# Performance work log

Measured on AMD Instinct MI355X. Metric: run time of the kernel, lower is better.

The kernel has to match this reference:

```python
import jax, jax.numpy as jnp
from jax import lax
import numpy as np

B, N, H, T, NPB = 1024, 50, 128, 50, 3
C_TANH, NEG = 10.0, 1e9


def _lstm(x, h, c, Wi, Wh, b):
    gates = x @ Wi + h @ Wh + b
    i, f, g, o = jnp.split(gates, 4, axis=-1)
    c2 = jax.nn.sigmoid(f) * c + jax.nn.sigmoid(i) * jnp.tanh(g)
    return jax.nn.sigmoid(o) * jnp.tanh(c2), c2


def setup_inputs() -> dict:
    key = jax.random.key(0)
    ks = jax.random.split(key, 20)
    rn = lambda k, shape, fan: (jax.random.normal(k, shape, jnp.float32) / np.float32(np.sqrt(fan)))
    return {
        'input_pnt': jax.random.uniform(ks[0], (B, N, 2), jnp.float32),
        'W_emb': rn(ks[1], (2, H), 2), 'b_emb': jnp.zeros((H,), jnp.float32),
        'dec_init': rn(ks[2], (1, 1, H), H),
        'Wi': rn(ks[3], (H, 4 * H), H), 'Wh': rn(ks[4], (H, 4 * H), H), 'b_lstm': jnp.zeros((4 * H,), jnp.float32),
        'Wq_g': rn(ks[5], (H, H), H), 'Wref_g': rn(ks[6], (H, H), H), 'v_g': rn(ks[7], (H,), H),
        'Wq_p': rn(ks[8], (H, H), H), 'Wref_p': rn(ks[9], (H, H), H), 'v_p': rn(ks[10], (H,), H),
        'Wi_c': rn(ks[11], (H, 4 * H), H), 'Wh_c': rn(ks[12], (H, 4 * H), H), 'b_c': jnp.zeros((4 * H,), jnp.float32),
        'Wq_c': rn(ks[13], (H, H), H), 'Wref_c': rn(ks[14], (H, H), H), 'v_c': rn(ks[15], (H,), H),
        'W1': rn(ks[16], (H, H), H), 'b1': jnp.zeros((H,), jnp.float32),
        'W2': rn(ks[17], (H, 1), H), 'b2': jnp.zeros((1,), jnp.float32),
    }


def _forward(input_pnt, W_emb, b_emb, dec_init, Wi, Wh, b_lstm, Wq_g, Wref_g, v_g,
             Wq_p, Wref_p, v_p, Wi_c, Wh_c, b_c, Wq_c, Wref_c, v_c, W1, b1, W2, b2):
    context = input_pnt @ W_emb + b_emb                    # [B,N,H] embedded nodes
    e_g = context @ Wref_g                                  # glimpse keys (step-invariant, hoisted)
    e_p = context @ Wref_p                                  # pointer keys (hoisted)
    z = jnp.zeros((B, H), context.dtype)
    carry0 = (z, z, jnp.zeros((B, N), context.dtype), jnp.broadcast_to(dec_init[0, 0], (B, H)))

    def step(carry, _):
        h, c, mask, dec_in = carry
        h2, c2 = _lstm(dec_in, h, c, Wi, Wh, b_lstm)
        # glimpse attention (masked)
        q = h2 @ Wq_g
        u = jnp.einsum('bnh,h->bn', jnp.tanh(e_g + q[:, None, :]), v_g) - NEG * mask
        g = jnp.einsum('bn,bnh->bh', jax.nn.softmax(u, -1), e_g)
        # pointer attention with tanh exploration clipping (masked)
        u2 = jnp.einsum('bnh,h->bn', jnp.tanh(e_p + (g @ Wq_p)[:, None, :]), v_p)
        logit = C_TANH * jnp.tanh(u2) - NEG * mask
        logprob = jax.nn.log_softmax(logit, -1)
        prob = jax.nn.softmax(logit, -1)
        action = jnp.argmax(prob, -1)                       # greedy decode
        mask2 = jnp.maximum(mask, jax.nn.one_hot(action, N, dtype=mask.dtype))
        dec_next = jnp.take_along_axis(context, action[:, None, None], axis=1)[:, 0]
        coords = jnp.take_along_axis(input_pnt, action[:, None, None], axis=1)[:, 0]
        return (h2, c2, mask2, dec_next), (logprob, prob, action, coords)

    (_, _, _, dec_last), (logprobs, probs, actions, coords) = lax.scan(step, carry0, None, length=T)
    logprobs = jnp.transpose(logprobs, (1, 0, 2))           # [B,T,N]
    probs = jnp.transpose(probs, (1, 0, 2))
    actions = jnp.transpose(actions, (1, 0))                # [B,T]
    coords = jnp.transpose(coords, (1, 0, 2))               # [B,T,2] visited coordinates
    # reward: TSP tour length
    seg = coords[:, 1:] - coords[:, :-1]
    close = coords[:, 0] - coords[:, -1]
    R = jnp.sum(jnp.sqrt(jnp.sum(seg * seg, -1) + 1e-10), -1) + jnp.sqrt(jnp.sum(close * close, -1) + 1e-10)
    # critic: one LSTM step on last action broadcast to hidden, cn[0], then process blocks
    a4c = jnp.broadcast_to(actions[:, -1].astype(context.dtype)[:, None], (B, H))
    _, hy = _lstm(a4c, z, z, Wi_c, Wh_c, b_c)
    enc = dec_last[:, None, :]                              # context gathered at last action, [B,1,H]
    e_c = enc @ Wref_c
    for _ in range(NPB):
        u = jnp.einsum('bnh,h->bn', jnp.tanh(e_c + (hy @ Wq_c)[:, None, :]), v_c)
        hy = jnp.einsum('bn,bnh->bh', jax.nn.softmax(C_TANH * jnp.tanh(u), -1), e_c)
    v = (jax.nn.relu(hy @ W1 + b1) @ W2 + b2)[:, 0]
    return R, v, logprobs, actions, coords, probs


def reference(input_pnt, W_emb, b_emb, dec_init, Wi, Wh, b_lstm, Wq_g, Wref_g, v_g,
              Wq_p, Wref_p, v_p, Wi_c, Wh_c, b_c, Wq_c, Wref_c, v_c, W1, b1, W2, b2):
    return _forward(input_pnt, W_emb, b_emb, dec_init, Wi, Wh, b_lstm, Wq_g, Wref_g, v_g,
                    Wq_p, Wref_p, v_p, Wi_c, Wh_c, b_c, Wq_c, Wref_c, v_c, W1, b1, W2, b2)
```

## Files before the change

### kernel.cpp

```cpp
#include <hip/hip_runtime.h>
#include <math.h>

#define Bsz 1024
#define Npt 50
#define Hd 128
#define G4 512
#define Tt 50
#define NEGC 1000000000.0f
#define CTANH 10.0f
#define L2E 1.44269504088896340736f

#define OFF_R 0
#define OFF_V 1024
#define OFF_LP 2048
#define OFF_A 2562048
#define OFF_C 2613248
#define OFF_P 2715648

#define WS_TG 0
#define WS_TP 512
#define WS_TQ 1024
#define WS_A0 1536
#define WS_A1 2048
#define WS_A2 2560
#define WS_A3 3072
#define WS_CT 3584

typedef __attribute__((ext_vector_type(8))) short s16x8;
typedef __attribute__((ext_vector_type(4))) float fx4;

__device__ __forceinline__ float fexp2(float x) {
  float r;
  asm("v_exp_f32 %0, %1" : "=v"(r) : "v"(x));
  return r;
}

__device__ __forceinline__ float fsig(float x) {
  return __builtin_amdgcn_rcpf(1.0f + __expf(-x));
}

__device__ __forceinline__ float ftanh(float x) {
  float e = __expf(2.0f * x);
  return 1.0f - 2.0f * __builtin_amdgcn_rcpf(e + 1.0f);
}

__device__ __forceinline__ unsigned short f2bf(float x) {
  unsigned int u = __float_as_uint(x);
  unsigned int r = (u + 0x7fffu + ((u >> 16) & 1u)) >> 16;
  return (unsigned short)r;
}
__device__ __forceinline__ float bf2f(unsigned short b) {
  return __uint_as_float(((unsigned int)b) << 16);
}

__device__ __forceinline__ float dpp_sum_bcast(float x) {
  int v;
  v = __builtin_amdgcn_update_dpp(0, __float_as_int(x), 0x111, 0xf, 0xf, true);
  x += __int_as_float(v);
  v = __builtin_amdgcn_update_dpp(0, __float_as_int(x), 0x112, 0xf, 0xf, true);
  x += __int_as_float(v);
  v = __builtin_amdgcn_update_dpp(0, __float_as_int(x), 0x114, 0xf, 0xf, true);
  x += __int_as_float(v);
  v = __builtin_amdgcn_update_dpp(0, __float_as_int(x), 0x118, 0xf, 0xf, true);
  x += __int_as_float(v);
  v = __builtin_amdgcn_update_dpp(0, __float_as_int(x), 0x142, 0xf, 0xf, true);
  x += __int_as_float(v);
  v = __builtin_amdgcn_update_dpp(0, __float_as_int(x), 0x143, 0xf, 0xf, true);
  x += __int_as_float(v);
  return __int_as_float(__builtin_amdgcn_readlane(__float_as_int(x), 63));
}

__device__ __forceinline__ float dpp_max_bcast(float x) {
  int v;
  v = __builtin_amdgcn_update_dpp(0, __float_as_int(x), 0x111, 0xf, 0xf, true);
  x = fmaxf(x, __int_as_float(v));
  v = __builtin_amdgcn_update_dpp(0, __float_as_int(x), 0x112, 0xf, 0xf, true);
  x = fmaxf(x, __int_as_float(v));
  v = __builtin_amdgcn_update_dpp(0, __float_as_int(x), 0x114, 0xf, 0xf, true);
  x = fmaxf(x, __int_as_float(v));
  v = __builtin_amdgcn_update_dpp(0, __float_as_int(x), 0x118, 0xf, 0xf, true);
  x = fmaxf(x, __int_as_float(v));
  v = __builtin_amdgcn_update_dpp(0, __float_as_int(x), 0x142, 0xf, 0xf, true);
  x = fmaxf(x, __int_as_float(v));
  v = __builtin_amdgcn_update_dpp(0, __float_as_int(x), 0x143, 0xf, 0xf, true);
  x = fmaxf(x, __int_as_float(v));
  return __int_as_float(__builtin_amdgcn_readlane(__float_as_int(x), 63));
}

__device__ __forceinline__ float xsum(float x) {
  #pragma unroll
  for (int off = 32; off >= 1; off >>= 1) x += __shfl_xor(x, off, 64);
  return x;
}

__global__ __launch_bounds__(512) void k_pre(const float* __restrict__ Wemb,
                                             const float* __restrict__ bemb,
                                             const float* __restrict__ dinit,
                                             const float* __restrict__ Wi,
                                             const float* __restrict__ bl,
                                             const float* __restrict__ Wqp,
                                             const float* __restrict__ Wrg,
                                             const float* __restrict__ Wrp,
                                             const float* __restrict__ vg,
                                             const float* __restrict__ vp,
                                             const float* __restrict__ Wrc,
                                             const float* __restrict__ W1,
                                             const float* __restrict__ b1,
                                             const float* __restrict__ W2,
                                             float* __restrict__ ws) {
  __shared__ float mg_s[2][128], mp_s[2][128], cg_s[128], cp_s[128];
  __shared__ float pg_s[2][128], pc_s[128];
  __shared__ float r0_s[128], r1_s[128], rc_s[128];
  int t = threadIdx.x;
  if (t < 256) {
    int j = t >> 7, hh = t & 127;
    float ag = 0.f, ap = 0.f;
    for (int k = 0; k < 128; ++k) {
      float we = Wemb[j * 128 + k];
      ag = fmaf(we, Wrg[k * 128 + hh], ag);
      ap = fmaf(we, Wrp[k * 128 + hh], ap);
    }
    mg_s[j][hh] = ag; mp_s[j][hh] = ap;
  } else if (t < 384) {
    int hh = t & 127;
    float cgv = 0.f, cpv = 0.f;
    for (int k = 0; k < 128; ++k) {
      float be = bemb[k];
      cgv = fmaf(be, Wrg[k * 128 + hh], cgv);
      cpv = fmaf(be, Wrp[k * 128 + hh], cpv);
    }
    cg_s[hh] = cgv; cp_s[hh] = cpv;
  } else {
    int hh = t & 127;
    float a0 = 0.f, a1 = 0.f, ac = 0.f;
    for (int k = 0; k < 128; ++k) {
      float wr = Wrc[k * 128 + hh];
      a0 = fmaf(Wemb[k], wr, a0);
      a1 = fmaf(Wemb[128 + k], wr, a1);
      ac = fmaf(bemb[k], wr, ac);
    }
    r0_s[hh] = a0; r1_s[hh] = a1; rc_s[hh] = ac;
  }
  __syncthreads();
  if (t < 256) {
    int j = t >> 7, hh = t & 127;
    float pg = 0.f;
    for (int k = 0; k < 128; ++k) pg = fmaf(mg_s[j][k], Wqp[k * 128 + hh], pg);
    pg_s[j][hh] = pg;
  } else if (t < 384) {
    int hh = t & 127;
    float pcv = 0.f;
    for (int k = 0; k < 128; ++k) pcv = fmaf(cg_s[k], Wqp[k * 128 + hh], pcv);
    pc_s[hh] = pcv + cp_s[hh];
  } else {
    int hh = t & 127;
    float t0 = 0.f, t1 = 0.f, tc = 0.f;
    for (int k = 0; k < 128; ++k) {
      float w1 = W1[k * 128 + hh];
      t0 = fmaf(r0_s[k], w1, t0);
      t1 = fmaf(r1_s[k], w1, t1);
      tc = fmaf(rc_s[k], w1, tc);
    }
    float4* w4 = (float4*)ws;
    w4[WS_CT / 4 + hh] = make_float4(t0, t1, tc + b1[hh], W2[hh]);
  }
  __syncthreads();
  if (t < 128) {
    float4* w4 = (float4*)ws;
    w4[WS_TG / 4 + t] = make_float4(mg_s[0][t], mg_s[1][t], vg[t], cg_s[t]);
    w4[WS_TP / 4 + t] = make_float4(mp_s[0][t], mp_s[1][t], vp[t], cp_s[t]);
    w4[WS_TQ / 4 + t] = make_float4(pg_s[0][t], pg_s[1][t], pc_s[t], 0.f);
  }
  {
    int j = t;
    float a0 = 0.f, a1 = 0.f, a2 = 0.f, a3 = 0.f;
    for (int k = 0; k < 128; ++k) {
      float wi = Wi[k * G4 + j];
      a0 = fmaf(Wemb[k], wi, a0);
      a1 = fmaf(Wemb[128 + k], wi, a1);
      a2 = fmaf(bemb[k], wi, a2);
      a3 = fmaf(dinit[k], wi, a3);
    }
    ws[WS_A0 + j] = a0;
    ws[WS_A1 + j] = a1;
    ws[WS_A2 + j] = a2 + bl[j];
    ws[WS_A3 + j] = a3 + bl[j];
  }
}

__global__ __launch_bounds__(1024, 4) void k_mega(const float* __restrict__ ip,
                                                  const float* __restrict__ Wh,
                                                  const float* __restrict__ Wqg,
                                                  const float* __restrict__ b2,
                                                  const float* __restrict__ ws,
                                                  float* __restrict__ out) {
  __shared__ __align__(16) float gates_s[4][G4];
  __shared__ s16x8 afrag_s[4][2][64];
  __shared__ __align__(16) float qpart[8][4][Hd];
  __shared__ __align__(16) float4 rowt_s[4][132];
  __shared__ __align__(16) float up_s[4][5][64];
  __shared__ __align__(16) float up2_s[4][5][64];
  __shared__ __align__(16) float h_s[4][Hd];
  __shared__ __align__(16) float c_s[4][Hd];
  __shared__ __align__(16) float tg_s[G4];
  __shared__ __align__(16) float tp_s[G4];
  __shared__ __align__(16) float tq_s[G4];
  __shared__ __align__(16) float ct_s[G4];
  __shared__ __align__(16) float a0_s[G4], a1_s[G4], a2_s[G4], a3_s[G4];
  __shared__ float vt_s[2];
  __shared__ __align__(16) float ip_s[4][Npt * 2];
  __shared__ float mask_s[4][Npt];
  __shared__ float ch_s[4][Npt * 2];
  __shared__ float sel_s[4][2];
  __shared__ int ctr_s[4];

  int t = threadIdx.x, blk = blockIdx.x;
  int w = t >> 6, lane = t & 63;
  int kh = t >> 7, jt = t & 127;
  int k0q = kh * 16;

  s16x8 Bh[2][4], Bl[2][4];
  {
    int cb = (w << 5) + (lane & 15);
    int g8 = (lane >> 4) << 3;
    #pragma unroll
    for (int tt = 0; tt < 2; ++tt)
      #pragma unroll
      for (int ks = 0; ks < 4; ++ks)
        #pragma unroll
        for (int j = 0; j < 8; ++j) {
          float x = Wh[(size_t)((ks << 5) + g8 + j) * G4 + cb + (tt << 4)];
          unsigned short hb = f2bf(x);
          Bh[tt][ks][j] = (short)hb;
          Bl[tt][ks][j] = (short)f2bf(x - bf2f(hb));
        }
  }
  float wqr[16];
  #pragma unroll
  for (int j = 0; j < 16; ++j)
    wqr[j] = Wqg[(kh * 16 + j) * Hd + jt];

  const float4* ws4 = (const float4*)ws;
  if (t < 128) {
    float4 g4 = ws4[WS_TG / 4 + t];
    ((float4*)tg_s)[t] = make_float4(2.f * L2E * g4.x, 2.f * L2E * g4.y,
                                     -2.f * g4.z, 2.f * L2E * g4.w);
    float4 p4 = ws4[WS_TP / 4 + t];
    ((float4*)tp_s)[t] = make_float4(2.f * L2E * p4.x, 2.f * L2E * p4.y,
                                     -2.f * p4.z, 0.f);
    float4 q4 = ws4[WS_TQ / 4 + t];
    ((float4*)tq_s)[t] = make_float4(2.f * L2E * q4.x, 2.f * L2E * q4.y,
                                     2.f * L2E * q4.z, 0.f);
    ((float4*)ct_s)[t] = ws4[WS_CT / 4 + t];
  } else if (t < 256) {
    int i = t - 128;
    ((float4*)a0_s)[i] = ((const float4*)(ws + WS_A0))[i];
    ((float4*)a1_s)[i] = ((const float4*)(ws + WS_A1))[i];
    ((float4*)a2_s)[i] = ((const float4*)(ws + WS_A2))[i];
    ((float4*)a3_s)[i] = ((const float4*)(ws + WS_A3))[i];
  }
  if (t < 200) {
    ((float2*)ip_s)[t] = ((const float2*)ip)[blk * 200 + t];
    ((float*)mask_s)[t] = 0.f;
  }
  if (t < 512) {
    int r = t >> 7, hh = t & 127;
    h_s[r][hh] = 0.f;
    c_s[r][hh] = 0.f;
  }
  ((float2*)gates_s)[t] = make_float2(0.f, 0.f);
  if (t < 2) {
    float sv = 0.f;
    for (int hp = 0; hp < 128; ++hp)
      sv += ws[(t ? WS_TP : WS_TG) + hp * 4 + 2];
    vt_s[t] = sv;
  }
  if (t < 16) {
    rowt_s[t >> 2][128 + (t & 3)] = make_float4(0.f, 0.f, 0.f, 0.f);
  }
  if (t < 8) ((float*)sel_s)[t] = 0.f;
  if (t < 4) ctr_s[t] = 0;
  __syncthreads();

  int cr = w & 3, hc = w >> 2;
  int ell = hc * 64 + lane;
  int rep = ell / 50;
  bool act = ell < 250;
  int n2 = ell - rep * 50;
  int h0 = rep * 26;
  float2 pw = make_float2(0.f, 0.f);
  if (act) pw = ((float2*)ip_s)[cr * Npt + n2];

  int lt = 0;
  auto lsync = [&]() {
    lt += 4;
    if (lane == 0)
      __hip_atomic_fetch_add(&ctr_s[cr], 1, __ATOMIC_RELEASE,
                             __HIP_MEMORY_SCOPE_WORKGROUP);
    while (__hip_atomic_load(&ctr_s[cr], __ATOMIC_ACQUIRE,
                             __HIP_MEMORY_SCOPE_WORKGROUP) < lt)
      __builtin_amdgcn_s_sleep(1);
  };

  for (int s = 0; s < Tt; ++s) {
    __syncthreads();
    if (t < 512) {
      int r = t >> 7, hh = t & 127;
      float p0 = sel_s[r][0], p1 = sel_s[r][1];
      float g[4];
      #pragma unroll
      for (int gi = 0; gi < 4; ++gi) {
        int j = gi * 128 + hh;
        float x = (s == 0) ? a3_s[j]
                           : fmaf(p0, a0_s[j], fmaf(p1, a1_s[j], a2_s[j]));
        g[gi] = x + gates_s[r][j];
      }
      float c2 = fsig(g[1]) * c_s[r][hh] + fsig(g[0]) * ftanh(g[2]);
      float h2 = fsig(g[3]) * ftanh(c2);
      c_s[r][hh] = c2;
      h_s[r][hh] = h2;
    }
    __syncthreads();
    {
      #pragma unroll
      for (int r = 0; r < 4; ++r) {
        float hv[16];
        #pragma unroll
        for (int q4i = 0; q4i < 4; ++q4i)
          *(float4*)&hv[q4i * 4] = *(const float4*)&h_s[r][k0q + q4i * 4];
        float a = 0.f;
        #pragma unroll
        for (int kk = 0; kk < 16; ++kk) a = fmaf(hv[kk], wqr[kk], a);
        qpart[kh][r][jt] = a;
      }
      if (s + 1 < Tt && w >= 8 && w < 12) {
        int ks = w - 8, row = lane & 15, g8 = (lane >> 4) << 3;
        float xv[8];
        if (row < 4) {
          const float* hp8 = &h_s[row][(ks << 5) + g8];
          *(float4*)&xv[0] = *(const float4*)hp8;
          *(float4*)&xv[4] = *(const float4*)(hp8 + 4);
        } else {
          #pragma unroll
          for (int j = 0; j < 8; ++j) xv[j] = 0.f;
        }
        s16x8 hf, lf;
        #pragma unroll
        for (int j = 0; j < 8; ++j) {
          unsigned short hb = f2bf(xv[j]);
          hf[j] = (short)hb;
          lf[j] = (short)f2bf(xv[j] - bf2f(hb));
        }
        afrag_s[ks][0][lane] = hf;
        afrag_s[ks][1][lane] = lf;
      }
    }
    __syncthreads();
    if (lane < 32) {
      int h = hc * 32 + lane;
      float4 tg4 = ((float4*)tg_s)[h];
      float qs = tg4.w + 2.f * L2E *
                 (qpart[0][cr][h] + qpart[1][cr][h] + qpart[2][cr][h]
                + qpart[3][cr][h] + qpart[4][cr][h] + qpart[5][cr][h]
                + qpart[6][cr][h] + qpart[7][cr][h]);
      rowt_s[cr][h] = make_float4(tg4.x, tg4.y, qs, tg4.z);
    }
    lsync();
    if (act) {
      float ac = 0.f;
      #pragma unroll 13
      for (int i = 0; i < 26; ++i) {
        float4 f4 = rowt_s[cr][h0 + i];
        float a = fmaf(pw.x, f4.x, fmaf(pw.y, f4.y, f4.z));
        ac = fmaf(f4.w, __builtin_amdgcn_rcpf(fexp2(a) + 1.0f), ac);
      }
      up_s[cr][rep][n2] = ac;
    }
    lsync();
    {
      float u = vt_s[0] + up_s[cr][0][lane] + up_s[cr][1][lane]
              + up_s[cr][2][lane] + up_s[cr][3][lane] + up_s[cr][4][lane];
      float e = 0.f;
      if (lane < Npt) e = __expf(u - NEGC * mask_s[cr][lane]);
      float ssum = dpp_sum_bcast(e);
      float sx = dpp_sum_bcast(e * pw.x * 0.f + e * ((float2*)ip_s)[cr * Npt + (lane < Npt ? lane : 0)].x * (lane < Npt ? 1.f : 0.f));
      float sy = dpp_sum_bcast(e * ((float2*)ip_s)[cr * Npt + (lane < Npt ? lane : 0)].y * (lane < Npt ? 1.f : 0.f));
      float inv = __builtin_amdgcn_rcpf(ssum);
      float s0 = sx * inv;
      float s1 = sy * inv;
      if (lane < 32) {
        int h = hc * 32 + lane;
        float4 tq4 = ((float4*)tq_s)[h];
        float4 tp4 = ((float4*)tp_s)[h];
        float qs2 = fmaf(s0, tq4.x, fmaf(s1, tq4.y, tq4.z));
        rowt_s[cr][h] = make_float4(tp4.x, tp4.y, qs2, tp4.z);
      }
    }
    lsync();
    if (act) {
      float ac = 0.f;
      #pragma unroll 13
      for (int i = 0; i < 26; ++i) {
        float4 f4 = rowt_s[cr][h0 + i];
        float a = fmaf(pw.x, f4.x, fmaf(pw.y, f4.y, f4.z));
        ac = fmaf(f4.w, __builtin_amdgcn_rcpf(fexp2(a) + 1.0f), ac);
      }
      up2_s[cr][rep][n2] = ac;
    }
    lsync();
    if (hc == 3) {
      int row = cr, b = blk * 4 + row;
      float u = vt_s[1] + up2_s[row][0][lane] + up2_s[row][1][lane]
              + up2_s[row][2][lane] + up2_s[row][3][lane]
              + up2_s[row][4][lane];
      float x = 0.f, e = 0.f;
      if (lane < Npt) {
        x = CTANH * ftanh(u) - NEGC * mask_s[row][lane];
        e = __expf(x);
      }
      float ssum = dpp_sum_bcast(e);
      float ls = __logf(ssum);
      float prob = e * __builtin_amdgcn_rcpf(ssum);
      if (lane < Npt) {
        out[OFF_LP + ((size_t)b * Tt + s) * Npt + lane] = x - ls;
        out[OFF_P + ((size_t)b * Tt + s) * Npt + lane] = prob;
      }
      float mx = dpp_max_bcast(prob);
      unsigned long long bal = __ballot((prob == mx) && (lane < Npt));
      int a = __ffsll(bal) - 1;
      float p0a = ip_s[row][2 * a];
      float p1a = ip_s[row][2 * a + 1];
      if (lane == 0) {
        out[OFF_A + (size_t)b * Tt + s] = (float)a;
        out[OFF_C + ((size_t)b * Tt + s) * 2 + 0] = p0a;
        out[OFF_C + ((size_t)b * Tt + s) * 2 + 1] = p1a;
        ((float2*)ch_s)[row * Npt + s] = make_float2(p0a, p1a);
        mask_s[row][a] = 1.0f;
        sel_s[row][0] = p0a;
        sel_s[row][1] = p1a;
      }
    }
    if (s + 1 < Tt) {
      fx4 d0 = {0.f, 0.f, 0.f, 0.f}, d1 = {0.f, 0.f, 0.f, 0.f};
      #pragma unroll
      for (int ks = 0; ks < 4; ++ks) {
        s16x8 ah = afrag_s[ks][0][lane];
        s16x8 al = afrag_s[ks][1][lane];
        d0 = __builtin_amdgcn_mfma_f32_16x16x32_bf16(ah, Bh[0][ks], d0, 0, 0, 0);
        d0 = __builtin_amdgcn_mfma_f32_16x16x32_bf16(ah, Bl[0][ks], d0, 0, 0, 0);
        d0 = __builtin_amdgcn_mfma_f32_16x16x32_bf16(al, Bh[0][ks], d0, 0, 0, 0);
        d0 = __builtin_amdgcn_mfma_f32_16x16x32_bf16(al, Bl[0][ks], d0, 0, 0, 0);
        d1 = __builtin_amdgcn_mfma_f32_16x16x32_bf16(ah, Bh[1][ks], d1, 0, 0, 0);
        d1 = __builtin_amdgcn_mfma_f32_16x16x32_bf16(ah, Bl[1][ks], d1, 0, 0, 0);
        d1 = __builtin_amdgcn_mfma_f32_16x16x32_bf16(al, Bh[1][ks], d1, 0, 0, 0);
        d1 = __builtin_amdgcn_mfma_f32_16x16x32_bf16(al, Bl[1][ks], d1, 0, 0, 0);
      }
      if (lane < 16) {
        int c0 = (w << 5) + lane;
        #pragma unroll
        for (int rr = 0; rr < 4; ++rr) {
          gates_s[rr][c0] = d0[rr];
          gates_s[rr][c0 + 16] = d1[rr];
        }
      }
    }
  }
  __syncthreads();

  if (w < 4) {
    int r = w, b = blk * 4 + r;
    float p0 = sel_s[r][0], p1 = sel_s[r][1];
    float4 ct0 = ((float4*)ct_s)[lane];
    float4 ct1 = ((float4*)ct_s)[64 + lane];
    float t1a = fmaxf(fmaf(p0, ct0.x, fmaf(p1, ct0.y, ct0.z)), 0.f);
    float t1b = fmaxf(fmaf(p0, ct1.x, fmaf(p1, ct1.y, ct1.z)), 0.f);
    float sv = xsum(t1a * ct0.w + t1b * ct1.w);
    if (lane == 0) out[OFF_V + b] = sv + b2[0];
    float rr = 0.f;
    if (lane < Npt) {
      float2 c0 = ((float2*)ch_s)[r * Npt + lane];
      float2 c1 = ((float2*)ch_s)[r * Npt + ((lane == Npt - 1) ? 0 : lane + 1)];
      float dx = c1.x - c0.x, dy = c1.y - c0.y;
      rr = sqrtf(dx * dx + dy * dy + 1e-10f);
    }
    rr = xsum(rr);
    if (lane == 0) out[OFF_R + b] = rr;
  }
}

extern "C" void kernel_launch(void* const* d_in, const int* in_sizes, int n_in,
                              void* d_out, int out_size, void* d_ws, size_t ws_size,
                              hipStream_t stream) {
  (void)in_sizes; (void)n_in; (void)out_size; (void)ws_size;
  const float* ip    = (const float*)d_in[0];
  const float* Wemb  = (const float*)d_in[1];
  const float* bemb  = (const float*)d_in[2];
  const float* dinit = (const float*)d_in[3];
  const float* Wi    = (const float*)d_in[4];
  const float* Wh    = (const float*)d_in[5];
  const float* bl    = (const float*)d_in[6];
  const float* Wqg   = (const float*)d_in[7];
  const float* Wrg   = (const float*)d_in[8];
  const float* vg    = (const float*)d_in[9];
  const float* Wqp   = (const float*)d_in[10];
  const float* Wrp   = (const float*)d_in[11];
  const float* vp    = (const float*)d_in[12];
  const float* Wrc   = (const float*)d_in[17];
  const float* W1    = (const float*)d_in[19];
  const float* b1    = (const float*)d_in[20];
  const float* W2    = (const float*)d_in[21];
  const float* b2    = (const float*)d_in[22];
  float* out = (float*)d_out;
  float* ws  = (float*)d_ws;

  k_pre<<<1, 512, 0, stream>>>(Wemb, bemb, dinit, Wi, bl, Wqp, Wrg, Wrp,
                               vg, vp, Wrc, W1, b1, W2, ws);
  k_mega<<<256, 1024, 0, stream>>>(ip, Wh, Wqg, b2, ws, out);
}
```

Measured before the change: 562.2 us.

## Compute glimpse query via split-bf16 MFMA and hoist gate MFMAs earlier

The LSTM step now writes h directly into bf16 hi/lo MFMA A-fragments instead of an fp32 h buffer. The glimpse query projection h@Wq_g moves from a per-thread FMA reduction with an 8-way partial sum to split-bf16 MFMAs on 8 waves, writing straight into a persistent per-row table. The recurrent h@Wh gate MFMAs move ahead of the attention phases, with d0/d1 interleaved and stored at the end of the step. Separate glimpse and pointer tables drop one lsync, the qpart reduction and per-step table rebuilds, at the cost of more live registers holding the Wq fragments.

```diff
diff --git a/kernel.cpp b/kernel.cpp
--- a/kernel.cpp
+++ b/kernel.cpp
@@ -9,6 +9,7 @@
 #define NEGC 1000000000.0f
 #define CTANH 10.0f
 #define L2E 1.44269504088896340736f
+#define TL2E (2.0f * L2E)
 
 #define OFF_R 0
 #define OFF_V 1024
@@ -196,14 +197,12 @@
                                                   float* __restrict__ out) {
   __shared__ __align__(16) float gates_s[4][G4];
   __shared__ s16x8 afrag_s[4][2][64];
-  __shared__ __align__(16) float qpart[8][4][Hd];
-  __shared__ __align__(16) float4 rowt_s[4][132];
+  __shared__ __align__(16) float4 rowtg_s[4][132];
+  __shared__ __align__(16) float4 rowtp_s[4][132];
   __shared__ __align__(16) float up_s[4][5][64];
   __shared__ __align__(16) float up2_s[4][5][64];
-  __shared__ __align__(16) float h_s[4][Hd];
   __shared__ __align__(16) float c_s[4][Hd];
-  __shared__ __align__(16) float tg_s[G4];
-  __shared__ __align__(16) float tp_s[G4];
+  __shared__ float tgw_s[Hd];
   __shared__ __align__(16) float tq_s[G4];
   __shared__ __align__(16) float ct_s[G4];
   __shared__ __align__(16) float a0_s[G4], a1_s[G4], a2_s[G4], a3_s[G4];
@@ -216,8 +215,6 @@
 
   int t = threadIdx.x, blk = blockIdx.x;
   int w = t >> 6, lane = t & 63;
-  int kh = t >> 7, jt = t & 127;
-  int k0q = kh * 16;
 
   s16x8 Bh[2][4], Bl[2][4];
   {
@@ -235,22 +232,27 @@
           Bl[tt][ks][j] = (short)f2bf(x - bf2f(hb));
         }
   }
-  float wqr[16];
-  #pragma unroll
-  for (int j = 0; j < 16; ++j)
-    wqr[j] = Wqg[(kh * 16 + j) * Hd + jt];
+  s16x8 Bqh[4], Bql[4];
+  if (w < 8) {
+    int cb = (w << 4) + (lane & 15);
+    int g8 = (lane >> 4) << 3;
+    #pragma unroll
+    for (int ks = 0; ks < 4; ++ks)
+      #pragma unroll
+      for (int j = 0; j < 8; ++j) {
+        float x = Wqg[(size_t)((ks << 5) + g8 + j) * Hd + cb];
+        unsigned short hb = f2bf(x);
+        Bqh[ks][j] = (short)hb;
+        Bql[ks][j] = (short)f2bf(x - bf2f(hb));
+      }
+  }
 
   const float4* ws4 = (const float4*)ws;
   if (t < 128) {
     float4 g4 = ws4[WS_TG / 4 + t];
-    ((float4*)tg_s)[t] = make_float4(2.f * L2E * g4.x, 2.f * L2E * g4.y,
-                                     -2.f * g4.z, 2.f * L2E * g4.w);
-    float4 p4 = ws4[WS_TP / 4 + t];
-    ((float4*)tp_s)[t] = make_float4(2.f * L2E * p4.x, 2.f * L2E * p4.y,
-                                     -2.f * p4.z, 0.f);
+    tgw_s[t] = TL2E * g4.w;
     float4 q4 = ws4[WS_TQ / 4 + t];
-    ((float4*)tq_s)[t] = make_float4(2.f * L2E * q4.x, 2.f * L2E * q4.y,
-                                     2.f * L2E * q4.z, 0.f);
+    ((float4*)tq_s)[t] = make_float4(TL2E * q4.x, TL2E * q4.y, TL2E * q4.z, 0.f);
     ((float4*)ct_s)[t] = ws4[WS_CT / 4 + t];
   } else if (t < 256) {
     int i = t - 128;
@@ -259,16 +261,20 @@
     ((float4*)a2_s)[i] = ((const float4*)(ws + WS_A2))[i];
     ((float4*)a3_s)[i] = ((const float4*)(ws + WS_A3))[i];
   }
+  if (t < 512) {
+    int r = t >> 7, hh = t & 127;
+    float4 g4 = ws4[WS_TG / 4 + hh];
+    rowtg_s[r][hh] = make_float4(TL2E * g4.x, TL2E * g4.y, 0.f, -2.f * g4.z);
+    float4 p4 = ws4[WS_TP / 4 + hh];
+    rowtp_s[r][hh] = make_float4(TL2E * p4.x, TL2E * p4.y, 0.f, -2.f * p4.z);
+    c_s[r][hh] = 0.f;
+    ((s16x8*)afrag_s)[t] = (s16x8)(short)0;
+  }
+  ((float2*)gates_s)[t] = make_float2(0.f, 0.f);
   if (t < 200) {
     ((float2*)ip_s)[t] = ((const float2*)ip)[blk * 200 + t];
     ((float*)mask_s)[t] = 0.f;
   }
-  if (t < 512) {
-    int r = t >> 7, hh = t & 127;
-    h_s[r][hh] = 0.f;
-    c_s[r][hh] = 0.f;
-  }
-  ((float2*)gates_s)[t] = make_float2(0.f, 0.f);
   if (t < 2) {
     float sv = 0.f;
     for (int hp = 0; hp < 128; ++hp)
@@ -276,7 +282,8 @@
     vt_s[t] = sv;
   }
   if (t < 16) {
-    rowt_s[t >> 2][128 + (t & 3)] = make_float4(0.f, 0.f, 0.f, 0.f);
+    rowtg_s[t >> 2][128 + (t & 3)] = make_float4(0.f, 0.f, 0.f, 0.f);
+    rowtp_s[t >> 2][128 + (t & 3)] = make_float4(0.f, 0.f, 0.f, 0.f);
   }
   if (t < 8) ((float*)sel_s)[t] = 0.f;
   if (t < 4) ctr_s[t] = 0;
@@ -290,6 +297,8 @@
   int h0 = rep * 26;
   float2 pw = make_float2(0.f, 0.f);
   if (act) pw = ((float2*)ip_s)[cr * Npt + n2];
+  float2 pnl = make_float2(0.f, 0.f);
+  if (lane < Npt) pnl = ((float2*)ip_s)[cr * Npt + lane];
 
   int lt = 0;
   auto lsync = [&]() {
@@ -318,59 +327,55 @@
       float c2 = fsig(g[1]) * c_s[r][hh] + fsig(g[0]) * ftanh(g[2]);
       float h2 = fsig(g[3]) * ftanh(c2);
       c_s[r][hh] = c2;
-      h_s[r][hh] = h2;
+      int ks = hh >> 5, gg = (hh >> 3) & 3, j = hh & 7, la = gg * 16 + r;
+      unsigned short hb = f2bf(h2);
+      ((short*)&afrag_s[ks][0][la])[j] = (short)hb;
+      ((short*)&afrag_s[ks][1][la])[j] = (short)f2bf(h2 - bf2f(hb));
     }
     __syncthreads();
+    fx4 d0 = {0.f, 0.f, 0.f, 0.f}, d1 = {0.f, 0.f, 0.f, 0.f};
     {
-      #pragma unroll
-      for (int r = 0; r < 4; ++r) {
-        float hv[16];
+      if (w < 8) {
+        fx4 qd = {0.f, 0.f, 0.f, 0.f};
         #pragma unroll
-        for (int q4i = 0; q4i < 4; ++q4i)
-          *(float4*)&hv[q4i * 4] = *(const float4*)&h_s[r][k0q + q4i * 4];
-        float a = 0.f;
+        for (int ks = 0; ks < 4; ++ks) {
+          s16x8 ah = afrag_s[ks][0][lane];
+          s16x8 al = afrag_s[ks][1][lane];
+          qd = __builtin_amdgcn_mfma_f32_16x16x32_bf16(ah, Bqh[ks], qd, 0, 0, 0);
+          qd = __builtin_amdgcn_mfma_f32_16x16x32_bf16(ah, Bql[ks], qd, 0, 0, 0);
+          qd = __builtin_amdgcn_mfma_f32_16x16x32_bf16(al, Bqh[ks], qd, 0, 0, 0);
+          qd = __builtin_amdgcn_mfma_f32_16x16x32_bf16(al, Bql[ks], qd, 0, 0, 0);
+        }
+        if (lane < 16) {
+          int hcol = (w << 4) + lane;
+          float tw = tgw_s[hcol];
+          #pragma unroll
+          for (int rr = 0; rr < 4; ++rr)
+            ((float*)&rowtg_s[rr][hcol])[2] = fmaf(TL2E, qd[rr], tw);
+        }
+      }
+      if (s + 1 < Tt) {
         #pragma unroll
-        for (int kk = 0; kk < 16; ++kk) a = fmaf(hv[kk], wqr[kk], a);
-        qpart[kh][r][jt] = a;
-      }
-      if (s + 1 < Tt && w >= 8 && w < 12) {
-        int ks = w - 8, row = lane & 15, g8 = (lane >> 4) << 3;
-        float xv[8];
-        if (row < 4) {
-          const float* hp8 = &h_s[row][(ks << 5) + g8];
-          *(float4*)&xv[0] = *(const float4*)hp8;
-          *(float4*)&xv[4] = *(const float4*)(hp8 + 4);
-        } else {
-          #pragma unroll
-          for (int j = 0; j < 8; ++j) xv[j] = 0.f;
+        for (int ks = 0; ks < 4; ++ks) {
+          s16x8 ah = afrag_s[ks][0][lane];
+          s16x8 al = afrag_s[ks][1][lane];
+          d0 = __builtin_amdgcn_mfma_f32_16x16x32_bf16(ah, Bh[0][ks], d0, 0, 0, 0);
+          d1 = __builtin_amdgcn_mfma_f32_16x16x32_bf16(ah, Bh[1][ks], d1, 0, 0, 0);
+          d0 = __builtin_amdgcn_mfma_f32_16x16x32_bf16(ah, Bl[0][ks], d0, 0, 0, 0);
+          d1 = __builtin_amdgcn_mfma_f32_16x16x32_bf16(ah, Bl[1][ks], d1, 0, 0, 0);
+          d0 = __builtin_amdgcn_mfma_f32_16x16x32_bf16(al, Bh[0][ks], d0, 0, 0, 0);
+          d1 = __builtin_amdgcn_mfma_f32_16x16x32_bf16(al, Bh[1][ks], d1, 0, 0, 0);
+          d0 = __builtin_amdgcn_mfma_f32_16x16x32_bf16(al, Bl[0][ks], d0, 0, 0, 0);
+          d1 = __builtin_amdgcn_mfma_f32_16x16x32_bf16(al, Bl[1][ks], d1, 0, 0, 0);
         }
-        s16x8 hf, lf;
-        #pragma unroll
-        for (int j = 0; j < 8; ++j) {
-          unsigned short hb = f2bf(xv[j]);
-          hf[j] = (short)hb;
-          lf[j] = (short)f2bf(xv[j] - bf2f(hb));
-        }
-        afrag_s[ks][0][lane] = hf;
-        afrag_s[ks][1][lane] = lf;
       }
     }
     __syncthreads();
-    if (lane < 32) {
-      int h = hc * 32 + lane;
-      float4 tg4 = ((float4*)tg_s)[h];
-      float qs = tg4.w + 2.f * L2E *
-                 (qpart[0][cr][h] + qpart[1][cr][h] + qpart[2][cr][h]
-                + qpart[3][cr][h] + qpart[4][cr][h] + qpart[5][cr][h]
-                + qpart[6][cr][h] + qpart[7][cr][h]);
-      rowt_s[cr][h] = make_float4(tg4.x, tg4.y, qs, tg4.z);
-    }
-    lsync();
     if (act) {
       float ac = 0.f;
       #pragma unroll 13
       for (int i = 0; i < 26; ++i) {
-        float4 f4 = rowt_s[cr][h0 + i];
+        float4 f4 = rowtg_s[cr][h0 + i];
         float a = fmaf(pw.x, f4.x, fmaf(pw.y, f4.y, f4.z));
         ac = fmaf(f4.w, __builtin_amdgcn_rcpf(fexp2(a) + 1.0f), ac);
       }
@@ -383,17 +388,16 @@
       float e = 0.f;
       if (lane < Npt) e = __expf(u - NEGC * mask_s[cr][lane]);
       float ssum = dpp_sum_bcast(e);
-      float sx = dpp_sum_bcast(e * pw.x * 0.f + e * ((float2*)ip_s)[cr * Npt + (lane < Npt ? lane : 0)].x * (lane < Npt ? 1.f : 0.f));
-      float sy = dpp_sum_bcast(e * ((float2*)ip_s)[cr * Npt + (lane < Npt ? lane : 0)].y * (lane < Npt ? 1.f : 0.f));
+      float sx = dpp_sum_bcast(e * pnl.x);
+      float sy = dpp_sum_bcast(e * pnl.y);
       float inv = __builtin_amdgcn_rcpf(ssum);
       float s0 = sx * inv;
       float s1 = sy * inv;
       if (lane < 32) {
         int h = hc * 32 + lane;
         float4 tq4 = ((float4*)tq_s)[h];
-        float4 tp4 = ((float4*)tp_s)[h];
         float qs2 = fmaf(s0, tq4.x, fmaf(s1, tq4.y, tq4.z));
-        rowt_s[cr][h] = make_float4(tp4.x, tp4.y, qs2, tp4.z);
+        ((float*)&rowtp_s[cr][h])[2] = qs2;
       }
     }
     lsync();
@@ -401,7 +405,7 @@
       float ac = 0.f;
       #pragma unroll 13
       for (int i = 0; i < 26; ++i) {
-        float4 f4 = rowt_s[cr][h0 + i];
+        float4 f4 = rowtp_s[cr][h0 + i];
         float a = fmaf(pw.x, f4.x, fmaf(pw.y, f4.y, f4.z));
         ac = fmaf(f4.w, __builtin_amdgcn_rcpf(fexp2(a) + 1.0f), ac);
       }
@@ -440,28 +444,12 @@
         sel_s[row][1] = p1a;
       }
     }
-    if (s + 1 < Tt) {
-      fx4 d0 = {0.f, 0.f, 0.f, 0.f}, d1 = {0.f, 0.f, 0.f, 0.f};
+    if (s + 1 < Tt && lane < 16) {
+      int c0 = (w << 5) + lane;
       #pragma unroll
-      for (int ks = 0; ks < 4; ++ks) {
-        s16x8 ah = afrag_s[ks][0][lane];
-        s16x8 al = afrag_s[ks][1][lane];
-        d0 = __builtin_amdgcn_mfma_f32_16x16x32_bf16(ah, Bh[0][ks], d0, 0, 0, 0);
-        d0 = __builtin_amdgcn_mfma_f32_16x16x32_bf16(ah, Bl[0][ks], d0, 0, 0, 0);
-        d0 = __builtin_amdgcn_mfma_f32_16x16x32_bf16(al, Bh[0][ks], d0, 0, 0, 0);
-        d0 = __builtin_amdgcn_mfma_f32_16x16x32_bf16(al, Bl[0][ks], d0, 0, 0, 0);
-        d1 = __builtin_amdgcn_mfma_f32_16x16x32_bf16(ah, Bh[1][ks], d1, 0, 0, 0);
-        d1 = __builtin_amdgcn_mfma_f32_16x16x32_bf16(ah, Bl[1][ks], d1, 0, 0, 0);
-        d1 = __builtin_amdgcn_mfma_f32_16x16x32_bf16(al, Bh[1][ks], d1, 0, 0, 0);
-        d1 = __builtin_amdgcn_mfma_f32_16x16x32_bf16(al, Bl[1][ks], d1, 0, 0, 0);
-      }
-      if (lane < 16) {
-        int c0 = (w << 5) + lane;
-        #pragma unroll
-        for (int rr = 0; rr < 4; ++rr) {
-          gates_s[rr][c0] = d0[rr];
-          gates_s[rr][c0 + 16] = d1[rr];
-        }
+      for (int rr = 0; rr < 4; ++rr) {
+        gates_s[rr][c0] = d0[rr];
+        gates_s[rr][c0 + 16] = d1[rr];
       }
     }
   }
```

Measured after the change: 562.2 us. Within noise of the previous version (+0.0%).

## Drop per-row barriers via wave-local attention tables and split post/wait sync

Applied to the files above, without the earlier changes.

Each wave now builds its own private slice of the glimpse and pointer attention tables (wtg_s/wtp_s) instead of a shared per-row table. This removes two of the four intra-row counter barriers per step. The barrier is split into post and wait halves so that only the argmax wave waits before the final softmax. The recurrent MFMA gate product moves earlier, and its results are written while other waves wait, so matrix work overlaps the attention phases. The cost is redundant table construction per wave and more shared memory.

```diff
diff --git a/kernel.cpp b/kernel.cpp
--- a/kernel.cpp
+++ b/kernel.cpp
@@ -9,6 +9,7 @@
 #define NEGC 1000000000.0f
 #define CTANH 10.0f
 #define L2E 1.44269504088896340736f
+#define TL2E (2.0f * L2E)
 
 #define OFF_R 0
 #define OFF_V 1024
@@ -196,14 +197,15 @@
                                                   float* __restrict__ out) {
   __shared__ __align__(16) float gates_s[4][G4];
   __shared__ s16x8 afrag_s[4][2][64];
+  __shared__ __align__(16) float4 tg_inv[132];
+  __shared__ __align__(16) float4 tp_inv[132];
+  __shared__ __align__(16) float4 wtg_s[16][52];
+  __shared__ __align__(16) float4 wtp_s[16][52];
   __shared__ __align__(16) float qpart[8][4][Hd];
-  __shared__ __align__(16) float4 rowt_s[4][132];
   __shared__ __align__(16) float up_s[4][5][64];
   __shared__ __align__(16) float up2_s[4][5][64];
   __shared__ __align__(16) float h_s[4][Hd];
   __shared__ __align__(16) float c_s[4][Hd];
-  __shared__ __align__(16) float tg_s[G4];
-  __shared__ __align__(16) float tp_s[G4];
   __shared__ __align__(16) float tq_s[G4];
   __shared__ __align__(16) float ct_s[G4];
   __shared__ __align__(16) float a0_s[G4], a1_s[G4], a2_s[G4], a3_s[G4];
@@ -243,11 +245,11 @@
   const float4* ws4 = (const float4*)ws;
   if (t < 128) {
     float4 g4 = ws4[WS_TG / 4 + t];
-    ((float4*)tg_s)[t] = make_float4(2.f * L2E * g4.x, 2.f * L2E * g4.y,
-                                     -2.f * g4.z, 2.f * L2E * g4.w);
+    tg_inv[t] = make_float4(2.f * L2E * g4.x, 2.f * L2E * g4.y,
+                            2.f * L2E * g4.w, -2.f * g4.z);
     float4 p4 = ws4[WS_TP / 4 + t];
-    ((float4*)tp_s)[t] = make_float4(2.f * L2E * p4.x, 2.f * L2E * p4.y,
-                                     -2.f * p4.z, 0.f);
+    tp_inv[t] = make_float4(2.f * L2E * p4.x, 2.f * L2E * p4.y,
+                            0.f, -2.f * p4.z);
     float4 q4 = ws4[WS_TQ / 4 + t];
     ((float4*)tq_s)[t] = make_float4(2.f * L2E * q4.x, 2.f * L2E * q4.y,
                                      2.f * L2E * q4.z, 0.f);
@@ -275,8 +277,9 @@
       sv += ws[(t ? WS_TP : WS_TG) + hp * 4 + 2];
     vt_s[t] = sv;
   }
-  if (t < 16) {
-    rowt_s[t >> 2][128 + (t & 3)] = make_float4(0.f, 0.f, 0.f, 0.f);
+  if (t < 4) {
+    tg_inv[128 + t] = make_float4(0.f, 0.f, 0.f, 0.f);
+    tp_inv[128 + t] = make_float4(0.f, 0.f, 0.f, 0.f);
   }
   if (t < 8) ((float*)sel_s)[t] = 0.f;
   if (t < 4) ctr_s[t] = 0;
@@ -287,16 +290,21 @@
   int rep = ell / 50;
   bool act = ell < 250;
   int n2 = ell - rep * 50;
-  int h0 = rep * 26;
+  int baseh = 26 * ((hc * 64) / 50);
+  int idxb = rep * 26 - baseh;
   float2 pw = make_float2(0.f, 0.f);
   if (act) pw = ((float2*)ip_s)[cr * Npt + n2];
+  float2 pnl = make_float2(0.f, 0.f);
+  if (lane < Npt) pnl = ((float2*)ip_s)[cr * Npt + lane];
 
   int lt = 0;
-  auto lsync = [&]() {
+  auto lpost = [&]() {
     lt += 4;
     if (lane == 0)
       __hip_atomic_fetch_add(&ctr_s[cr], 1, __ATOMIC_RELEASE,
                              __HIP_MEMORY_SCOPE_WORKGROUP);
+  };
+  auto lwait = [&]() {
     while (__hip_atomic_load(&ctr_s[cr], __ATOMIC_ACQUIRE,
                              __HIP_MEMORY_SCOPE_WORKGROUP) < lt)
       __builtin_amdgcn_s_sleep(1);
@@ -356,59 +364,92 @@
       }
     }
     __syncthreads();
-    if (lane < 32) {
-      int h = hc * 32 + lane;
-      float4 tg4 = ((float4*)tg_s)[h];
-      float qs = tg4.w + 2.f * L2E *
-                 (qpart[0][cr][h] + qpart[1][cr][h] + qpart[2][cr][h]
-                + qpart[3][cr][h] + qpart[4][cr][h] + qpart[5][cr][h]
-                + qpart[6][cr][h] + qpart[7][cr][h]);
-      rowt_s[cr][h] = make_float4(tg4.x, tg4.y, qs, tg4.z);
-    }
-    lsync();
+    fx4 d0 = {0.f, 0.f, 0.f, 0.f}, d1 = {0.f, 0.f, 0.f, 0.f};
+    if (s + 1 < Tt) {
+      #pragma unroll
+      for (int ks = 0; ks < 4; ++ks) {
+        s16x8 ah = afrag_s[ks][0][lane];
+        s16x8 al = afrag_s[ks][1][lane];
+        d0 = __builtin_amdgcn_mfma_f32_16x16x32_bf16(ah, Bh[0][ks], d0, 0, 0, 0);
+        d0 = __builtin_amdgcn_mfma_f32_16x16x32_bf16(ah, Bl[0][ks], d0, 0, 0, 0);
+        d0 = __builtin_amdgcn_mfma_f32_16x16x32_bf16(al, Bh[0][ks], d0, 0, 0, 0);
+        d0 = __builtin_amdgcn_mfma_f32_16x16x32_bf16(al, Bl[0][ks], d0, 0, 0, 0);
+        d1 = __builtin_amdgcn_mfma_f32_16x16x32_bf16(ah, Bh[1][ks], d1, 0, 0, 0);
+        d1 = __builtin_amdgcn_mfma_f32_16x16x32_bf16(ah, Bl[1][ks], d1, 0, 0, 0);
+        d1 = __builtin_amdgcn_mfma_f32_16x16x32_bf16(al, Bh[1][ks], d1, 0, 0, 0);
+        d1 = __builtin_amdgcn_mfma_f32_16x16x32_bf16(al, Bl[1][ks], d1, 0, 0, 0);
+      }
+    }
+    {
+      int hw = baseh + lane;
+      if (lane < 52) {
+        if (hw < 128) {
+          float4 iv = tg_inv[hw];
+          float qs = iv.z + 2.f * L2E *
+                     (qpart[0][cr][hw] + qpart[1][cr][hw] + qpart[2][cr][hw]
+                    + qpart[3][cr][hw] + qpart[4][cr][hw] + qpart[5][cr][hw]
+                    + qpart[6][cr][hw] + qpart[7][cr][hw]);
+          wtg_s[w][lane] = make_float4(iv.x, iv.y, qs, iv.w);
+        } else {
+          wtg_s[w][lane] = make_float4(0.f, 0.f, 0.f, 0.f);
+        }
+      }
+    }
     if (act) {
       float ac = 0.f;
       #pragma unroll 13
       for (int i = 0; i < 26; ++i) {
-        float4 f4 = rowt_s[cr][h0 + i];
+        float4 f4 = wtg_s[w][idxb + i];
         float a = fmaf(pw.x, f4.x, fmaf(pw.y, f4.y, f4.z));
         ac = fmaf(f4.w, __builtin_amdgcn_rcpf(fexp2(a) + 1.0f), ac);
       }
       up_s[cr][rep][n2] = ac;
     }
-    lsync();
+    lpost(); lwait();
     {
       float u = vt_s[0] + up_s[cr][0][lane] + up_s[cr][1][lane]
               + up_s[cr][2][lane] + up_s[cr][3][lane] + up_s[cr][4][lane];
       float e = 0.f;
       if (lane < Npt) e = __expf(u - NEGC * mask_s[cr][lane]);
       float ssum = dpp_sum_bcast(e);
-      float sx = dpp_sum_bcast(e * pw.x * 0.f + e * ((float2*)ip_s)[cr * Npt + (lane < Npt ? lane : 0)].x * (lane < Npt ? 1.f : 0.f));
-      float sy = dpp_sum_bcast(e * ((float2*)ip_s)[cr * Npt + (lane < Npt ? lane : 0)].y * (lane < Npt ? 1.f : 0.f));
+      float sx = dpp_sum_bcast(e * pnl.x);
+      float sy = dpp_sum_bcast(e * pnl.y);
       float inv = __builtin_amdgcn_rcpf(ssum);
       float s0 = sx * inv;
       float s1 = sy * inv;
-      if (lane < 32) {
-        int h = hc * 32 + lane;
-        float4 tq4 = ((float4*)tq_s)[h];
-        float4 tp4 = ((float4*)tp_s)[h];
-        float qs2 = fmaf(s0, tq4.x, fmaf(s1, tq4.y, tq4.z));
-        rowt_s[cr][h] = make_float4(tp4.x, tp4.y, qs2, tp4.z);
-      }
-    }
-    lsync();
+      int hw = baseh + lane;
+      if (lane < 52) {
+        if (hw < 128) {
+          float4 iv = tp_inv[hw];
+          float4 tq4 = ((float4*)tq_s)[hw];
+          float qs2 = fmaf(s0, tq4.x, fmaf(s1, tq4.y, tq4.z));
+          wtp_s[w][lane] = make_float4(iv.x, iv.y, qs2, iv.w);
+        } else {
+          wtp_s[w][lane] = make_float4(0.f, 0.f, 0.f, 0.f);
+        }
+      }
+    }
     if (act) {
       float ac = 0.f;
       #pragma unroll 13
       for (int i = 0; i < 26; ++i) {
-        float4 f4 = rowt_s[cr][h0 + i];
+        float4 f4 = wtp_s[w][idxb + i];
         float a = fmaf(pw.x, f4.x, fmaf(pw.y, f4.y, f4.z));
         ac = fmaf(f4.w, __builtin_amdgcn_rcpf(fexp2(a) + 1.0f), ac);
       }
       up2_s[cr][rep][n2] = ac;
     }
-    lsync();
+    lpost();
+    if (s + 1 < Tt && lane < 16) {
+      int c0 = (w << 5) + lane;
+      #pragma unroll
+      for (int rr = 0; rr < 4; ++rr) {
+        gates_s[rr][c0] = d0[rr];
+        gates_s[rr][c0 + 16] = d1[rr];
+      }
+    }
     if (hc == 3) {
+      lwait();
       int row = cr, b = blk * 4 + row;
       float u = vt_s[1] + up2_s[row][0][lane] + up2_s[row][1][lane]
               + up2_s[row][2][lane] + up2_s[row][3][lane]
@@ -438,30 +479,6 @@
         mask_s[row][a] = 1.0f;
         sel_s[row][0] = p0a;
         sel_s[row][1] = p1a;
-      }
-    }
-    if (s + 1 < Tt) {
-      fx4 d0 = {0.f, 0.f, 0.f, 0.f}, d1 = {0.f, 0.f, 0.f, 0.f};
-      #pragma unroll
-      for (int ks = 0; ks < 4; ++ks) {
-        s16x8 ah = afrag_s[ks][0][lane];
-        s16x8 al = afrag_s[ks][1][lane];
-        d0 = __builtin_amdgcn_mfma_f32_16x16x32_bf16(ah, Bh[0][ks], d0, 0, 0, 0);
-        d0 = __builtin_amdgcn_mfma_f32_16x16x32_bf16(ah, Bl[0][ks], d0, 0, 0, 0);
-        d0 = __builtin_amdgcn_mfma_f32_16x16x32_bf16(al, Bh[0][ks], d0, 0, 0, 0);
-        d0 = __builtin_amdgcn_mfma_f32_16x16x32_bf16(al, Bl[0][ks], d0, 0, 0, 0);
-        d1 = __builtin_amdgcn_mfma_f32_16x16x32_bf16(ah, Bh[1][ks], d1, 0, 0, 0);
-        d1 = __builtin_amdgcn_mfma_f32_16x16x32_bf16(ah, Bl[1][ks], d1, 0, 0, 0);
-        d1 = __builtin_amdgcn_mfma_f32_16x16x32_bf16(al, Bh[1][ks], d1, 0, 0, 0);
-        d1 = __builtin_amdgcn_mfma_f32_16x16x32_bf16(al, Bl[1][ks], d1, 0, 0, 0);
-      }
-      if (lane < 16) {
-        int c0 = (w << 5) + lane;
-        #pragma unroll
-        for (int rr = 0; rr < 4; ++rr) {
-          gates_s[rr][c0] = d0[rr];
-          gates_s[rr][c0 + 16] = d1[rr];
-        }
       }
     }
   }
```

Measured after the change: 599.8 us. +6.7%, slower.
